# Optimization experiments

Measured on AMD Instinct MI355X. Metric: run time of the kernel, lower is better.

## Reference

```python
import jax, jax.numpy as jnp
import numpy as np

BLOCK_SIZE = 64  # weights per (scale, zero_point) block along in_features


def _dequant(q_weights, q_scales, q_zp):
    # q_weights: [N, K] int codes in [0,16); q_scales/q_zp: [N, K//BLOCK_SIZE]
    N, K = q_weights.shape
    nb = K // BLOCK_SIZE
    q = q_weights.reshape(N, nb, BLOCK_SIZE).astype(q_scales.dtype)
    zp = q_zp.reshape(N, nb, 1).astype(q_scales.dtype)
    s = q_scales.reshape(N, nb, 1)
    return ((q - zp) * s).reshape(N, K)  # [N, K] float


def setup_inputs() -> dict:
    key = jax.random.key(0)
    k1, k2, k3, k4, k5 = jax.random.split(key, 5)
    M, K, N = 4096, 4096, 11008
    nb = K // BLOCK_SIZE
    return {
        "input": jax.random.normal(k1, (M, K), dtype=jnp.float32),
        "q_weights": jax.random.randint(k2, (N, K), 0, 16, dtype=jnp.int32),
        "q_scales": jax.random.uniform(k3, (N, nb), dtype=jnp.float32, minval=0.01, maxval=0.05),
        "q_zp": jax.random.randint(k4, (N, nb), 0, 16, dtype=jnp.int32),
        "bias": jax.random.normal(k5, (N,), dtype=jnp.float32),
    }


def reference(input, q_weights, q_scales, q_zp, bias):
    # Blockwise int4 dequant + GEMM: out[m, n] = sum_k input[m, k] * w[n, k]
    w = _dequant(q_weights, q_scales, q_zp)          # [N, K]
    out = jnp.einsum("mk,nk->mn", input, w)          # [M, N]
    return out + bias[None, :]
```

## Files before the change

kernel.cpp:

```cpp
#include <hip/hip_runtime.h>


#define BM 128
#define BN 128
#define BK 64
#define LDSN 72

typedef __attribute__((ext_vector_type(8))) short bf16x8;
typedef __attribute__((ext_vector_type(4))) float f32x4;

__device__ __forceinline__ unsigned short f2bf(float f) {
    union { float f; unsigned int u; } v; v.f = f;
    unsigned int u = v.u;
    u += 0x7FFFu + ((u >> 16) & 1u);
    return (unsigned short)(u >> 16);
}
__device__ __forceinline__ unsigned int pack2(float a, float b) {
    return (unsigned int)f2bf(a) | ((unsigned int)f2bf(b) << 16);
}

__device__ __forceinline__ void gl_lds16(const void* gp, void* lp) {
    __builtin_amdgcn_global_load_lds(
        (const __attribute__((address_space(1))) unsigned int*)gp,
        (__attribute__((address_space(3))) unsigned int*)lp,
        16, 0, 0);
}

__global__ __launch_bounds__(256)
void a2bf_kernel(const float* __restrict__ A, unsigned short* __restrict__ Ab,
                 long total4)
{
    long t = (long)blockIdx.x * blockDim.x + threadIdx.x;
    if (t >= total4) return;
    float4 v = ((const float4*)A)[t];
    uint2 p; p.x = pack2(v.x, v.y); p.y = pack2(v.z, v.w);
    ((uint2*)Ab)[t] = p;
}

__global__ __launch_bounds__(256)
void dequant_kernel(const int* __restrict__ Q, const float* __restrict__ S,
                    const int* __restrict__ Zp, unsigned short* __restrict__ W,
                    int K, int nb)
{
    const int n = blockIdx.y;
    const int k = (blockIdx.x * 256 + threadIdx.x) * 8;
    if (k >= K) return;
    const int kb = k >> 6;
    const float s  = S[(size_t)n * nb + kb];
    const float zs = (float)Zp[(size_t)n * nb + kb] * s;
    const int4* qp = (const int4*)(Q + (size_t)n * K + k);
    int4 q0 = qp[0], q1 = qp[1];
    uint4 o;
    o.x = pack2((float)q0.x * s - zs, (float)q0.y * s - zs);
    o.y = pack2((float)q0.z * s - zs, (float)q0.w * s - zs);
    o.z = pack2((float)q1.x * s - zs, (float)q1.y * s - zs);
    o.w = pack2((float)q1.z * s - zs, (float)q1.w * s - zs);
    *(uint4*)(W + (size_t)n * K + k) = o;
}

__global__ __launch_bounds__(256, 2)
void gemm_bt_kernel(const unsigned short* __restrict__ Ab,
                    const unsigned short* __restrict__ Wb,
                    const float* __restrict__ bias, float* __restrict__ C,
                    int M, int N, int K)
{
    __shared__ __align__(16) unsigned short As[BM * BK];
    __shared__ __align__(16) unsigned short Bs[BN * BK];

    const int tid = threadIdx.x;
    const int m0  = blockIdx.x * BM;
    const int n0  = blockIdx.y * BN;

    const int lane = tid & 63;
    const int wave = tid >> 6;
    const int wm   = (wave >> 1) * 64;
    const int wn   = (wave & 1) * 64;
    const int fr   = lane & 15;
    const int quad = lane >> 4;
    const int sw   = fr & 7;

    f32x4 acc[4][4];
    #pragma unroll
    for (int i = 0; i < 4; ++i)
        #pragma unroll
        for (int j = 0; j < 4; ++j)
            acc[i][j] = (f32x4){0.f, 0.f, 0.f, 0.f};

    const int ktiles = K / BK;
    for (int kt = 0; kt < ktiles; ++kt) {
        const int k0 = kt * BK;
        #pragma unroll
        for (int i = 0; i < 4; ++i) {
            const int c    = i * 256 + tid;
            const int row  = c >> 3;
            const int g    = (c & 7) ^ (row & 7);
            const int cole = g * 8;
            gl_lds16(Ab + (size_t)(m0 + row) * K + k0 + cole, (char*)As + c * 16);
            gl_lds16(Wb + (size_t)(n0 + row) * K + k0 + cole, (char*)Bs + c * 16);
        }
        __syncthreads();

        #pragma unroll
        for (int ks = 0; ks < 2; ++ks) {
            bf16x8 af[4], bfg[4];
            #pragma unroll
            for (int i = 0; i < 4; ++i) {
                const int row = wm + i * 16 + fr;
                const int p   = (ks * 4 + quad) ^ sw;
                af[i] = *(const bf16x8*)&As[row * BK + p * 8];
            }
            #pragma unroll
            for (int j = 0; j < 4; ++j) {
                const int row = wn + j * 16 + fr;
                const int p   = (ks * 4 + quad) ^ sw;
                bfg[j] = *(const bf16x8*)&Bs[row * BK + p * 8];
            }
            #pragma unroll
            for (int i = 0; i < 4; ++i)
                #pragma unroll
                for (int j = 0; j < 4; ++j)
                    acc[i][j] = __builtin_amdgcn_mfma_f32_16x16x32_bf16(af[i], bfg[j], acc[i][j], 0, 0, 0);
        }
        __syncthreads();
    }

    #pragma unroll
    for (int j = 0; j < 4; ++j) {
        const int n = n0 + wn + j * 16 + fr;
        const float bv = bias[n];
        #pragma unroll
        for (int i = 0; i < 4; ++i) {
            const int mb = m0 + wm + i * 16 + quad * 4;
            #pragma unroll
            for (int r = 0; r < 4; ++r)
                C[(size_t)(mb + r) * N + n] = acc[i][j][r] + bv;
        }
    }
}

__global__ __launch_bounds__(256, 2)
void q4gemm_fused(const float* __restrict__ A, const int* __restrict__ Q,
                  const float* __restrict__ S, const int* __restrict__ Zp,
                  const float* __restrict__ bias, float* __restrict__ C,
                  int M, int N, int K, int nb)
{
    __shared__ __align__(16) unsigned short As[BM * LDSN];
    __shared__ __align__(16) unsigned short Bs[BN * LDSN];

    const int tid = threadIdx.x;
    const int m0  = blockIdx.x * BM;
    const int n0  = blockIdx.y * BN;
    const int srow = tid >> 4;
    const int scol = (tid & 15) << 2;
    const int lane = tid & 63;
    const int wave = tid >> 6;
    const int wm   = (wave >> 1) * 64;
    const int wn   = (wave & 1) * 64;
    const int fr   = lane & 15;
    const int quad = lane >> 4;

    f32x4 acc[4][4];
    #pragma unroll
    for (int i = 0; i < 4; ++i)
        #pragma unroll
        for (int j = 0; j < 4; ++j)
            acc[i][j] = (f32x4){0.f, 0.f, 0.f, 0.f};

    const int ktiles = K / BK;
    for (int kt = 0; kt < ktiles; ++kt) {
        const int k0 = kt * BK;
        #pragma unroll
        for (int i = 0; i < 8; ++i) {
            const int r = i * 16 + srow;
            const float4 v = *(const float4*)(A + (size_t)(m0 + r) * K + k0 + scol);
            uint2 p; p.x = pack2(v.x, v.y); p.y = pack2(v.z, v.w);
            *(uint2*)&As[r * LDSN + scol] = p;
        }
        #pragma unroll
        for (int i = 0; i < 8; ++i) {
            const int r = i * 16 + srow;
            const int n = n0 + r;
            const int4 q = *(const int4*)(Q + (size_t)n * K + k0 + scol);
            const float s  = S[(size_t)n * nb + kt];
            const float zs = (float)Zp[(size_t)n * nb + kt] * s;
            uint2 p;
            p.x = pack2((float)q.x * s - zs, (float)q.y * s - zs);
            p.y = pack2((float)q.z * s - zs, (float)q.w * s - zs);
            *(uint2*)&Bs[r * LDSN + scol] = p;
        }
        __syncthreads();
        #pragma unroll
        for (int ks = 0; ks < 2; ++ks) {
            bf16x8 af[4], bfg[4];
            #pragma unroll
            for (int i = 0; i < 4; ++i)
                af[i] = *(const bf16x8*)&As[(wm + i * 16 + fr) * LDSN + ks * 32 + quad * 8];
            #pragma unroll
            for (int j = 0; j < 4; ++j)
                bfg[j] = *(const bf16x8*)&Bs[(wn + j * 16 + fr) * LDSN + ks * 32 + quad * 8];
            #pragma unroll
            for (int i = 0; i < 4; ++i)
                #pragma unroll
                for (int j = 0; j < 4; ++j)
                    acc[i][j] = __builtin_amdgcn_mfma_f32_16x16x32_bf16(af[i], bfg[j], acc[i][j], 0, 0, 0);
        }
        __syncthreads();
    }
    #pragma unroll
    for (int j = 0; j < 4; ++j) {
        const int n = n0 + wn + j * 16 + fr;
        const float bv = bias[n];
        #pragma unroll
        for (int i = 0; i < 4; ++i) {
            const int mb = m0 + wm + i * 16 + quad * 4;
            #pragma unroll
            for (int r = 0; r < 4; ++r)
                C[(size_t)(mb + r) * N + n] = acc[i][j][r] + bv;
        }
    }
}

extern "C" void kernel_launch(void* const* d_in, const int* in_sizes, int n_in,
                              void* d_out, int out_size, void* d_ws, size_t ws_size,
                              hipStream_t stream) {
    const float* A    = (const float*)d_in[0];
    const int*   Q    = (const int*)d_in[1];
    const float* S    = (const float*)d_in[2];
    const int*   Zp   = (const int*)d_in[3];
    const float* bias = (const float*)d_in[4];
    float* C = (float*)d_out;

    const int N  = in_sizes[4];
    const int K  = in_sizes[1] / N;
    const int M  = in_sizes[0] / K;
    const int nb = in_sizes[2] / N;

    const size_t needA = (size_t)M * K * 2;
    const size_t needW = (size_t)N * K * 2;

    if (ws_size >= needA + needW) {
        unsigned short* Ab = (unsigned short*)d_ws;
        unsigned short* Wb = (unsigned short*)((char*)d_ws + needA);

        long total4 = (long)M * K / 4;
        a2bf_kernel<<<(unsigned)((total4 + 255) / 256), 256, 0, stream>>>(A, Ab, total4);

        dim3 dq_grid((K / 8 + 255) / 256, N);
        dequant_kernel<<<dq_grid, 256, 0, stream>>>(Q, S, Zp, Wb, K, nb);

        dim3 grid(M / BM, N / BN);
        gemm_bt_kernel<<<grid, dim3(256), 0, stream>>>(Ab, Wb, bias, C, M, N, K);
    } else {
        dim3 grid(M / BM, N / BN);
        q4gemm_fused<<<grid, dim3(256), 0, stream>>>(A, Q, S, Zp, bias, C, M, N, K, nb);
    }
}
```

Baseline: 686.9 us.

## Add 256x256-tile 8-wave bf16 GEMM with ping-pong LDS pipeline

Adds a new bf16 MFMA GEMM kernel with 256x256 output tiles, 512 threads and double-buffered, XOR-swizzled LDS filled by direct global-to-LDS loads. The K loop is hand-scheduled into quarter-tile phases that interleave LDS fragment reads, asynchronous stage loads, explicit vmcnt/lgkmcnt waits and barriers, and raises wave priority around the MFMA bursts. The aim is more data reuse per tile and overlap of memory traffic with matrix math. The cost is 128KB of LDS per block, which limits occupancy, and a coarser grid that may leave a tail wave on the CUs. The launch code uses this kernel when the shapes divide evenly and keeps the old kernel as the fallback.

```diff
diff --git a/kernel.cpp b/kernel.cpp
--- a/kernel.cpp
+++ b/kernel.cpp
@@ -58,6 +58,201 @@
     *(uint4*)(W + (size_t)n * K + k) = o;
 }
 
+
+#define G8_BARRIER() do { asm volatile("" ::: "memory");                    \
+    __builtin_amdgcn_s_barrier(); asm volatile("" ::: "memory"); } while (0)
+#define G8_VMCNT(n) asm volatile("s_waitcnt vmcnt(" #n ")" ::: "memory")
+#define G8_LGKM0()  do { asm volatile("s_waitcnt lgkmcnt(0)" ::: "memory"); \
+    __builtin_amdgcn_sched_barrier(0); } while (0)
+
+#define G8_STAGE(G, kt, h, base, b)                                          \
+  do {                                                                       \
+    const unsigned short* _s = (G) + (long)(kt) * 64 + (long)(h) * 128 * K;  \
+    gl_lds16(_s + aoff0, (base) + (b) * 32768 + (h) * 16384 + lds0);         \
+    gl_lds16(_s + aoff1, (base) + (b) * 32768 + (h) * 16384 + lds1);         \
+  } while (0)
+
+#define G8_LOAD_AF(b, mh)                                                    \
+  { _Pragma("unroll") for (int _i = 0; _i < 4; ++_i) {                       \
+      const int _ra = (mh) * 128 + arow + _i * 16;                           \
+      const char* _pa = AsB + (b) * 32768 + _ra * 128;                       \
+      af[_i][0] = *(const bf16x8*)(_pa + ck0);                               \
+      af[_i][1] = *(const bf16x8*)(_pa + ck1);                               \
+  } }
+
+#define G8_LOAD_BF(b, nh)                                                    \
+  { _Pragma("unroll") for (int _j = 0; _j < 2; ++_j) {                       \
+      const int _rb = (nh) * 128 + brow + _j * 16;                           \
+      const char* _pb = BsB + (b) * 32768 + _rb * 128;                       \
+      bfg[_j][0] = *(const bf16x8*)(_pb + ck0);                              \
+      bfg[_j][1] = *(const bf16x8*)(_pb + ck1);                              \
+  } }
+
+#define G8_MFMA(q)                                                           \
+  __builtin_amdgcn_s_setprio(1);                                             \
+  { _Pragma("unroll") for (int _i = 0; _i < 4; ++_i)                         \
+    _Pragma("unroll") for (int _j = 0; _j < 2; ++_j) {                       \
+      acc[q][_i][_j] = __builtin_amdgcn_mfma_f32_16x16x32_bf16(              \
+          af[_i][0], bfg[_j][0], acc[q][_i][_j], 0, 0, 0);                   \
+      acc[q][_i][_j] = __builtin_amdgcn_mfma_f32_16x16x32_bf16(              \
+          af[_i][1], bfg[_j][1], acc[q][_i][_j], 0, 0, 0);                   \
+  } }                                                                        \
+  __builtin_amdgcn_s_setprio(0);
+
+__global__ __launch_bounds__(512, 2)
+void gemm8_kernel(const unsigned short* __restrict__ Ab,
+                  const unsigned short* __restrict__ Wb,
+                  const float* __restrict__ bias, float* __restrict__ C,
+                  int M, int N, int K)
+{
+    __shared__ __align__(16) unsigned short As[2][256][64];
+    __shared__ __align__(16) unsigned short Bs[2][256][64];
+
+    const int tid  = threadIdx.x;
+    const int m0   = blockIdx.x * 256;
+    const int n0   = blockIdx.y * 256;
+    const int lane = tid & 63;
+    const int wave = tid >> 6;
+    const int ww   = wave >> 2;
+    const int wv   = wave & 3;
+    const int fr   = lane & 15;
+    const int quad = lane >> 4;
+    const int sw   = fr & 7;
+
+    const int rl0 = tid >> 3;
+    const int rl1 = (512 + tid) >> 3;
+    const int pp  = tid & 7;
+    const long aoff0 = (long)rl0 * K + (long)((pp ^ (rl0 & 7)) * 8);
+    const long aoff1 = (long)rl1 * K + (long)((pp ^ (rl1 & 7)) * 8);
+    const int lds0 = tid * 16;
+    const int lds1 = (512 + tid) * 16;
+
+    const int ck0 = (quad ^ sw) * 16;
+    const int ck1 = ((4 + quad) ^ sw) * 16;
+    const int arow = ww * 64 + fr;
+    const int brow = wv * 32 + fr;
+
+    char* AsB = (char*)&As[0][0][0];
+    char* BsB = (char*)&Bs[0][0][0];
+
+    const unsigned short* Ag = Ab + (size_t)m0 * K;
+    const unsigned short* Bg = Wb + (size_t)n0 * K;
+
+    f32x4 acc[4][4][2];
+    #pragma unroll
+    for (int q = 0; q < 4; ++q)
+        #pragma unroll
+        for (int i = 0; i < 4; ++i)
+            #pragma unroll
+            for (int j = 0; j < 2; ++j)
+                acc[q][i][j] = (f32x4){0.f, 0.f, 0.f, 0.f};
+
+    bf16x8 af[4][2], bfg[2][2];
+
+    G8_STAGE(Ag, 0, 0, AsB, 0);
+    G8_STAGE(Bg, 0, 0, BsB, 0);
+    G8_STAGE(Ag, 0, 1, AsB, 0);
+    G8_STAGE(Bg, 0, 1, BsB, 0);
+    G8_STAGE(Ag, 1, 0, AsB, 1);
+    G8_STAGE(Bg, 1, 0, BsB, 1);
+    G8_VMCNT(4);
+    G8_BARRIER();
+
+    const int nit = K / 128;
+    for (int it = 0; it < nit - 1; ++it) {
+        const int t = 2 * it;
+        G8_LOAD_AF(0, 0); G8_LOAD_BF(0, 0);
+        G8_STAGE(Ag, t + 1, 1, AsB, 1);
+        G8_BARRIER(); G8_LGKM0();
+        G8_MFMA(0);
+        G8_VMCNT(6);
+        G8_BARRIER();
+        G8_LOAD_BF(0, 1);
+        G8_STAGE(Bg, t + 1, 1, BsB, 1);
+        G8_BARRIER(); G8_LGKM0();
+        G8_MFMA(1);
+        G8_BARRIER();
+        G8_LOAD_AF(0, 1); G8_LOAD_BF(0, 0);
+        G8_STAGE(Ag, t + 2, 0, AsB, 0);
+        G8_BARRIER(); G8_LGKM0();
+        G8_MFMA(2);
+        G8_BARRIER();
+        G8_LOAD_BF(0, 1);
+        G8_STAGE(Bg, t + 2, 0, BsB, 0);
+        G8_BARRIER(); G8_LGKM0();
+        G8_MFMA(3);
+        G8_VMCNT(8);
+        G8_BARRIER();
+        G8_LOAD_AF(1, 0); G8_LOAD_BF(1, 0);
+        G8_STAGE(Ag, t + 2, 1, AsB, 0);
+        G8_BARRIER(); G8_LGKM0();
+        G8_MFMA(0);
+        G8_VMCNT(6);
+        G8_BARRIER();
+        G8_LOAD_BF(1, 1);
+        G8_STAGE(Bg, t + 2, 1, BsB, 0);
+        G8_BARRIER(); G8_LGKM0();
+        G8_MFMA(1);
+        G8_BARRIER();
+        G8_LOAD_AF(1, 1); G8_LOAD_BF(1, 0);
+        G8_STAGE(Ag, t + 3, 0, AsB, 1);
+        G8_BARRIER(); G8_LGKM0();
+        G8_MFMA(2);
+        G8_BARRIER();
+        G8_LOAD_BF(1, 1);
+        G8_STAGE(Bg, t + 3, 0, BsB, 1);
+        G8_BARRIER(); G8_LGKM0();
+        G8_MFMA(3);
+        G8_VMCNT(8);
+        G8_BARRIER();
+    }
+    {
+        const int t = 2 * (nit - 1);
+        G8_LOAD_AF(0, 0); G8_LOAD_BF(0, 0);
+        G8_STAGE(Ag, t + 1, 1, AsB, 1);
+        G8_BARRIER(); G8_LGKM0(); G8_MFMA(0); G8_VMCNT(6); G8_BARRIER();
+
+        G8_LOAD_BF(0, 1);
+        G8_STAGE(Bg, t + 1, 1, BsB, 1);
+        G8_BARRIER(); G8_LGKM0(); G8_MFMA(1); G8_BARRIER();
+
+        G8_LOAD_AF(0, 1); G8_LOAD_BF(0, 0);
+        G8_BARRIER(); G8_LGKM0(); G8_MFMA(2); G8_BARRIER();
+
+        G8_LOAD_BF(0, 1);
+        G8_BARRIER(); G8_LGKM0(); G8_MFMA(3); G8_VMCNT(4); G8_BARRIER();
+
+        G8_LOAD_AF(1, 0); G8_LOAD_BF(1, 0);
+        G8_BARRIER(); G8_LGKM0(); G8_MFMA(0); G8_VMCNT(0); G8_BARRIER();
+
+        G8_LOAD_BF(1, 1);
+        G8_BARRIER(); G8_LGKM0(); G8_MFMA(1); G8_BARRIER();
+
+        G8_LOAD_AF(1, 1); G8_LOAD_BF(1, 0);
+        G8_BARRIER(); G8_LGKM0(); G8_MFMA(2); G8_BARRIER();
+
+        G8_LOAD_BF(1, 1);
+        G8_BARRIER(); G8_LGKM0(); G8_MFMA(3); G8_BARRIER();
+    }
+
+    #pragma unroll
+    for (int q = 0; q < 4; ++q) {
+        const int mh = q >> 1, nh = q & 1;
+        #pragma unroll
+        for (int j = 0; j < 2; ++j) {
+            const int n = n0 + nh * 128 + brow + j * 16;
+            const float bv = bias[n];
+            #pragma unroll
+            for (int i = 0; i < 4; ++i) {
+                const int mb = m0 + mh * 128 + ww * 64 + i * 16 + quad * 4;
+                #pragma unroll
+                for (int r = 0; r < 4; ++r)
+                    C[(size_t)(mb + r) * N + n] = acc[q][i][j][r] + bv;
+            }
+        }
+    }
+}
+
 __global__ __launch_bounds__(256, 2)
 void gemm_bt_kernel(const unsigned short* __restrict__ Ab,
                     const unsigned short* __restrict__ Wb,
@@ -248,8 +443,13 @@
         dim3 dq_grid((K / 8 + 255) / 256, N);
         dequant_kernel<<<dq_grid, 256, 0, stream>>>(Q, S, Zp, Wb, K, nb);
 
-        dim3 grid(M / BM, N / BN);
-        gemm_bt_kernel<<<grid, dim3(256), 0, stream>>>(Ab, Wb, bias, C, M, N, K);
+        if ((M % 256) == 0 && (N % 256) == 0 && (K % 128) == 0 && K >= 256) {
+            dim3 grid(M / 256, N / 256);
+            gemm8_kernel<<<grid, dim3(512), 0, stream>>>(Ab, Wb, bias, C, M, N, K);
+        } else {
+            dim3 grid(M / BM, N / BN);
+            gemm_bt_kernel<<<grid, dim3(256), 0, stream>>>(Ab, Wb, bias, C, M, N, K);
+        }
     } else {
         dim3 grid(M / BM, N / BN);
         q4gemm_fused<<<grid, dim3(256), 0, stream>>>(A, Q, S, Zp, bias, C, M, N, K, nb);
```

Result: slower. 726.3 us (+5.7%).
